# Performance work log

Hardware: AMD Instinct MI355X
Metric: run time of the kernel (lower is better)

## Reference

```python
import jax, jax.numpy as jnp
import numpy as np

B, S, DM = 4, 2048, 1024
H, HD = 16, 64  # num_heads, head_dimension


def setup_inputs() -> dict:
    key = jax.random.key(0)
    ks = jax.random.split(key, 11)
    s = 0.02
    return {
        "queries": jax.random.normal(ks[0], (B, S, DM), dtype=jnp.float32),
        "keys": jax.random.normal(ks[1], (B, S, DM), dtype=jnp.float32),
        "values": jax.random.normal(ks[2], (B, S, DM), dtype=jnp.float32),
        # projection params, stored [in, out] (transpose of torch Linear weight)
        "Wq": jax.random.normal(ks[3], (DM, H * HD), dtype=jnp.float32) * s,
        "bq": jnp.zeros((H * HD,), dtype=jnp.float32),
        "Wk": jax.random.normal(ks[4], (DM, H * HD), dtype=jnp.float32) * s,
        "bk": jnp.zeros((H * HD,), dtype=jnp.float32),
        "Wv": jax.random.normal(ks[5], (DM, H * HD), dtype=jnp.float32) * s,
        "bv": jnp.zeros((H * HD,), dtype=jnp.float32),
        "Wo": jax.random.normal(ks[6], (H * HD, DM), dtype=jnp.float32) * s,
        "bo": jnp.zeros((DM,), dtype=jnp.float32),
    }


def reference(queries, keys, values, Wq, bq, Wk, bk, Wv, bv, Wo, bo):
    b, s, _ = queries.shape
    # project and split heads: [b, s, H*HD] -> [b, H, s, HD]
    def split(x):
        return x.reshape(b, s, H, HD).transpose(0, 2, 1, 3)
    q = split(queries @ Wq + bq)
    k = split(keys @ Wk + bk)
    v = split(values @ Wv + bv)
    # raw scores [b, H, sq, sk]
    attn = jnp.einsum("bhqd,bhkd->bhqk", q, k)
    # FAITHFUL to source: mask is a no-op (masked_fill result discarded);
    # softmax over axis=2 (the QUERY axis), then scaled by 1/sqrt(HD) after.
    attn = jax.nn.softmax(attn, axis=2) / jnp.sqrt(jnp.float32(HD))
    out = jnp.einsum("bhqk,bhkd->bhqd", attn, v)  # [b, H, s, HD]
    out = out.transpose(0, 2, 1, 3).reshape(b, s, H * HD)
    return out @ Wo + bo
```

## Files before the change

### kernel.cpp

```cpp
#include <hip/hip_runtime.h>
#include <cstddef>


typedef unsigned short u16t;
typedef __attribute__((ext_vector_type(8))) short short8;
typedef __attribute__((ext_vector_type(4))) float floatx4;
typedef __attribute__((ext_vector_type(4))) unsigned int uintx4;

#define MFMA16(a, b, c) __builtin_amdgcn_mfma_f32_16x16x32_bf16((a), (b), (c), 0, 0, 0)
#define GLDS16(g, l)                                                        \
  __builtin_amdgcn_global_load_lds(                                         \
      (const __attribute__((address_space(1))) unsigned int*)(g),           \
      (__attribute__((address_space(3))) unsigned int*)(l), 16, 0, 0)

#if __has_builtin(__builtin_amdgcn_exp2f)
#define EXP2(x) __builtin_amdgcn_exp2f(x)
#else
#define EXP2(x) __expf(0.69314718f * (x))
#endif

static __device__ __forceinline__ u16t f2bf(float f) {
  union { float f; unsigned u; } v; v.f = f;
  unsigned r = v.u + 0x7FFFu + ((v.u >> 16) & 1u);
  return (u16t)(r >> 16);
}
static __device__ __forceinline__ unsigned pack2(float hi, float lo) {
  union { float f; unsigned u; } a, b; a.f = hi; b.f = lo;
  return __builtin_amdgcn_perm(a.u + 0x8000u, b.u + 0x8000u, 0x07060302u);
}

static __device__ __forceinline__ int swz(int row, int col) {
  return (((col >> 3) ^ (row & 7)) << 3) | (col & 7);
}

#define SEQ    2048
#define NHEAD  16
#define HDIM   64
#define DMODEL 1024

__global__ __launch_bounds__(256)
void wt_kernel(const float* __restrict__ W0, const float* __restrict__ W1,
               const float* __restrict__ W2, const float* __restrict__ W3,
               u16t* __restrict__ T0, u16t* __restrict__ T1,
               u16t* __restrict__ T2, u16t* __restrict__ T3) {
  int id = blockIdx.x * 256 + threadIdx.x;
  int wsel = id >> 17;
  int r = id & 131071;
  int n = r & 1023;
  int k0 = (r >> 10) << 3;
  const float* W = wsel == 0 ? W0 : wsel == 1 ? W1 : wsel == 2 ? W2 : W3;
  u16t* T = wsel == 0 ? T0 : wsel == 1 ? T1 : wsel == 2 ? T2 : T3;
  const float* src = W + (size_t)k0 * 1024 + n;
  float f[8];
#pragma unroll
  for (int i = 0; i < 8; ++i) f[i] = src[(size_t)i * 1024];
  uint4 p;
  p.x = pack2(f[1], f[0]); p.y = pack2(f[3], f[2]);
  p.z = pack2(f[5], f[4]); p.w = pack2(f[7], f[6]);
  *(uint4*)&T[(size_t)n * 1024 + (k0 & ~63) + swz(n, k0 & 63)] = p;
}

__global__ __launch_bounds__(256)
void cvt_kernel(const float* __restrict__ X0, const float* __restrict__ X1,
                u16t* __restrict__ T0, u16t* __restrict__ T1) {
  int id = blockIdx.x * 256 + threadIdx.x;
  int wsel = id >> 20;
  int r = id & 1048575;
  int m = r >> 7;
  int k0 = (r & 127) << 3;
  const float* X = wsel == 0 ? X0 : X1;
  u16t* T = wsel == 0 ? T0 : T1;
  const float4* src = (const float4*)(X + (size_t)m * 1024 + k0);
  float4 a = src[0], b = src[1];
  uint4 p;
  p.x = pack2(a.y, a.x); p.y = pack2(a.w, a.z);
  p.z = pack2(b.y, b.x); p.w = pack2(b.w, b.z);
  *(uint4*)&T[(size_t)m * 1024 + (k0 & ~63) + swz(m, k0 & 63)] = p;
}

template <int MODE>
__global__ __launch_bounds__(256)
void gemm_bt(const void* __restrict__ Ap0, const void* __restrict__ Ap1,
             const u16t* __restrict__ BT0, const u16t* __restrict__ BT1,
             const float* __restrict__ bias0, const float* __restrict__ bias1,
             void* __restrict__ Cp0, void* __restrict__ Cp1,
             float sc0, float sc1, const float* __restrict__ sscv) {
  constexpr int K = 1024;
  __shared__ __align__(16) u16t lA[128 * 64];
  __shared__ __align__(16) u16t lB[128 * 64];
  const int z = blockIdx.z;
  const void* Ap = z ? Ap1 : Ap0;
  const u16t* BT = z ? BT1 : BT0;
  const float* bias = z ? bias1 : bias0;
  void* Cp = z ? Cp1 : Cp0;
  const float qsc = z ? sc1 : sc0;
  const int tid = threadIdx.x;
  const int lane = tid & 63, w = tid >> 6;
  const int wm = w >> 1, wn = w & 1;
  const int lrow = lane & 15, lq = lane >> 4;
  const int raw = blockIdx.y * 8 + blockIdx.x;
  const int xcd = raw & 7, slot = raw >> 3;
  const int m0 = (xcd * 8 + (slot >> 3)) * 128;
  const int n0 = (slot & 7) * 128;

  floatx4 acc[4][4];
#pragma unroll
  for (int i = 0; i < 4; ++i)
#pragma unroll
    for (int j = 0; j < 4; ++j) acc[i][j] = {0.f, 0.f, 0.f, 0.f};

  for (int kb = 0; kb < K; kb += 64) {
    if constexpr (MODE == 2) {
      const float* Ag = (const float*)Ap;
#pragma unroll
      for (int i = 0; i < 8; ++i) {
        int e = (i * 256 + tid) * 4;
        int r = e >> 6, c = e & 63;
        const float* src = Ag + (size_t)(m0 + r) * K + kb + c;
        uint2 p;
        p.x = pack2(src[1], src[0]);
        p.y = pack2(src[3], src[2]);
        *(uint2*)&lA[r * 64 + swz(r, c)] = p;
      }
    } else {
      const u16t* Ag = (const u16t*)Ap;
#pragma unroll
      for (int i = 0; i < 4; ++i) {
        int chunk = w * 4 + i;
        int off = chunk * 1024 + lane * 16;
        int r = off >> 7, ib = off & 127;
        GLDS16(Ag + (size_t)(m0 + r) * K + kb + (ib >> 1), &lA[chunk * 512]);
      }
    }
#pragma unroll
    for (int i = 0; i < 4; ++i) {
      int chunk = w * 4 + i;
      int off = chunk * 1024 + lane * 16;
      int r = off >> 7, ib = off & 127;
      GLDS16(BT + (size_t)(n0 + r) * K + kb + (ib >> 1), &lB[chunk * 512]);
    }
    __syncthreads();
#pragma unroll
    for (int kk = 0; kk < 2; ++kk) {
      short8 af[4], bfr[4];
#pragma unroll
      for (int t = 0; t < 4; ++t) {
        int ar = wm * 64 + t * 16 + lrow;
        af[t] = *(const short8*)&lA[ar * 64 + swz(ar, kk * 32 + lq * 8)];
      }
#pragma unroll
      for (int t = 0; t < 4; ++t) {
        int br = wn * 64 + t * 16 + lrow;
        bfr[t] = *(const short8*)&lB[br * 64 + swz(br, kk * 32 + lq * 8)];
      }
#pragma unroll
      for (int i = 0; i < 4; ++i)
#pragma unroll
        for (int j = 0; j < 4; ++j)
          acc[i][j] = MFMA16(af[i], bfr[j], acc[i][j]);
    }
    __syncthreads();
  }

  float bvv[4];
#pragma unroll
  for (int j = 0; j < 4; ++j) bvv[j] = bias[n0 + wn * 64 + j * 16 + lrow];
  const int h = (n0 + wn * 64) >> 6;
#pragma unroll
  for (int i = 0; i < 4; ++i) {
#pragma unroll
    for (int r = 0; r < 4; ++r) {
      int rg = m0 + wm * 64 + i * 16 + lq * 4 + r;
      int b = rg >> 11, s = rg & 2047;
      float rs;
      if constexpr (MODE == 2) rs = sscv[(size_t)(b * NHEAD + h) * SEQ + s];
      else                     rs = qsc;
#pragma unroll
      for (int j = 0; j < 4; ++j) {
        int cg = n0 + wn * 64 + j * 16 + lrow;
        float v = acc[i][j][r] + bvv[j];
        if constexpr (MODE == 1) {
          ((float*)Cp)[(size_t)rg * 1024 + cg] = v;
        } else {
          v *= rs;
          int d = cg & 63;
          size_t bh = (size_t)(b * NHEAD + h);
          if constexpr (MODE == 0) {
            ((u16t*)Cp)[(bh * SEQ + s) * HDIM + swz(s, d)] = f2bf(v);
          } else {
            int sp = (s & ~31) | (((s >> 2) & 3) << 3) | (s & 3) |
                     (((s >> 4) & 1) << 2);
            ((u16t*)Cp)[(bh * HDIM + d) * SEQ + (s & ~127) + swz(d, sp & 127)] =
                f2bf(v);
          }
        }
      }
    }
  }
}

__global__ __launch_bounds__(256)
void stats_kernel(const u16t* __restrict__ Qb, const u16t* __restrict__ Kb,
                  float* __restrict__ ss) {
  __shared__ __align__(16) u16t lK[128 * 64];
  __shared__ __align__(16) u16t lQ[128 * 64];
  const int tid = threadIdx.x, lane = tid & 63, w = tid >> 6;
  const int lrow = lane & 15, lq = lane >> 4;
  const int bh = blockIdx.x;
  const int c0 = blockIdx.y * 128;
  const u16t* Kbase = Kb + (size_t)bh * (SEQ * HDIM);
  const u16t* Qbase = Qb + (size_t)bh * (SEQ * HDIM);

#pragma unroll
  for (int i = 0; i < 4; ++i) {
    int chunk = w * 4 + i;
    GLDS16(Kbase + (size_t)c0 * HDIM + chunk * 512 + lane * 8, &lK[chunk * 512]);
  }

  short8 bfK[4];
  float lcur[2] = {0.f, 0.f};

  for (int q0 = 0; q0 < SEQ; q0 += 128) {
#pragma unroll
    for (int i = 0; i < 4; ++i) {
      int chunk = w * 4 + i;
      GLDS16(Qbase + (size_t)q0 * HDIM + chunk * 512 + lane * 8, &lQ[chunk * 512]);
    }
    __syncthreads();
    if (q0 == 0) {
#pragma unroll
      for (int nt = 0; nt < 2; ++nt) {
        int kr = w * 32 + nt * 16 + lrow;
        bfK[nt * 2]     = *(const short8*)&lK[kr * 64 + swz(kr, lq * 8)];
        bfK[nt * 2 + 1] = *(const short8*)&lK[kr * 64 + swz(kr, lq * 8 + 32)];
      }
    }
#pragma unroll
    for (int mt = 0; mt < 8; ++mt) {
      int qr = mt * 16 + lrow;
      short8 af0 = *(const short8*)&lQ[qr * 64 + swz(qr, lq * 8)];
      short8 af1 = *(const short8*)&lQ[qr * 64 + swz(qr, lq * 8 + 32)];
#pragma unroll
      for (int nt = 0; nt < 2; ++nt) {
        floatx4 a = {0.f, 0.f, 0.f, 0.f};
        a = MFMA16(af0, bfK[nt * 2], a);
        a = MFMA16(af1, bfK[nt * 2 + 1], a);
        lcur[nt] += EXP2(a[0]) + EXP2(a[1]) + EXP2(a[2]) + EXP2(a[3]);
      }
    }
    __syncthreads();
  }
#pragma unroll
  for (int t = 0; t < 2; ++t) {
    float ll = lcur[t];
    ll += __shfl_xor(ll, 16);
    ll += __shfl_xor(ll, 32);
    lcur[t] = ll;
  }
  if (lane < 16) {
#pragma unroll
    for (int t = 0; t < 2; ++t) {
      int col = c0 + w * 32 + t * 16 + lane;
      ss[(size_t)bh * SEQ + col] = 1.f / (8.f * lcur[t]);
    }
  }
}

__global__ __launch_bounds__(256)
void attn_kernel(const u16t* __restrict__ Qb, const u16t* __restrict__ Kb,
                 const u16t* __restrict__ Vt, u16t* __restrict__ Hout) {
  __shared__ __align__(16) u16t lK[128 * 64];
  __shared__ __align__(16) u16t lV[64 * 128];
  const int tid = threadIdx.x, lane = tid & 63, w = tid >> 6;
  const int lrow = lane & 15, lq = lane >> 4;
  const int bh = blockIdx.x, q0 = blockIdx.y * 128;
  const size_t hb = (size_t)bh * (SEQ * HDIM);

#pragma unroll
  for (int i = 0; i < 4; ++i) {
    int chunk = w * 4 + i;
    GLDS16(Qb + hb + (size_t)q0 * HDIM + chunk * 512 + lane * 8, &lK[chunk * 512]);
  }
  __syncthreads();
  short8 bq[2][2];
#pragma unroll
  for (int j = 0; j < 2; ++j) {
    int qr = w * 32 + j * 16 + lrow;
    bq[j][0] = *(const short8*)&lK[qr * 64 + swz(qr, lq * 8)];
    bq[j][1] = *(const short8*)&lK[qr * 64 + swz(qr, lq * 8 + 32)];
  }
  __syncthreads();

  floatx4 ao[2][4];
#pragma unroll
  for (int j = 0; j < 2; ++j)
#pragma unroll
    for (int t = 0; t < 4; ++t) ao[j][t] = {0.f, 0.f, 0.f, 0.f};

  for (int kt = 0; kt < 16; ++kt) {
    const int k0 = kt * 128;
#pragma unroll
    for (int i = 0; i < 4; ++i) {
      int chunk = w * 4 + i;
      GLDS16(Kb + hb + (size_t)k0 * HDIM + chunk * 512 + lane * 8, &lK[chunk * 512]);
    }
#pragma unroll
    for (int i = 0; i < 4; ++i) {
      int chunk = w * 4 + i;
      int off = chunk * 1024 + lane * 16;
      int d = off >> 8, ib = off & 255;
      GLDS16(Vt + hb + ((size_t)d << 11) + k0 + (ib >> 1), &lV[chunk * 512]);
    }
    __syncthreads();

#pragma unroll
    for (int kw = 0; kw < 4; ++kw) {
      short8 ak[2][2];
#pragma unroll
      for (int t = 0; t < 2; ++t) {
        int kr = (kw * 2 + t) * 16 + lrow;
        ak[t][0] = *(const short8*)&lK[kr * 64 + swz(kr, lq * 8)];
        ak[t][1] = *(const short8*)&lK[kr * 64 + swz(kr, lq * 8 + 32)];
      }
      short8 pa[2];
#pragma unroll
      for (int j = 0; j < 2; ++j) {
        floatx4 s0 = {0.f, 0.f, 0.f, 0.f}, s1 = {0.f, 0.f, 0.f, 0.f};
        s0 = MFMA16(ak[0][0], bq[j][0], s0);
        s0 = MFMA16(ak[0][1], bq[j][1], s0);
        s1 = MFMA16(ak[1][0], bq[j][0], s1);
        s1 = MFMA16(ak[1][1], bq[j][1], s1);
        uintx4 pw;
        pw[0] = pack2(EXP2(s0[1]), EXP2(s0[0]));
        pw[1] = pack2(EXP2(s0[3]), EXP2(s0[2]));
        pw[2] = pack2(EXP2(s1[1]), EXP2(s1[0]));
        pw[3] = pack2(EXP2(s1[3]), EXP2(s1[2]));
        pa[j] = __builtin_bit_cast(short8, pw);
      }
#pragma unroll
      for (int dt = 0; dt < 4; ++dt) {
        int vr = dt * 16 + lrow;
        short8 bv = *(const short8*)&lV[vr * 128 + swz(vr, kw * 32 + lq * 8)];
        ao[0][dt] = MFMA16(pa[0], bv, ao[0][dt]);
        ao[1][dt] = MFMA16(pa[1], bv, ao[1][dt]);
      }
    }
    __syncthreads();
  }

  const int b = bh >> 4, h = bh & 15;
#pragma unroll
  for (int j = 0; j < 2; ++j)
#pragma unroll
    for (int dt = 0; dt < 4; ++dt) {
      int d = dt * 16 + lrow;
#pragma unroll
      for (int r = 0; r < 4; ++r) {
        int q = q0 + w * 32 + j * 16 + lq * 4 + r;
        Hout[((size_t)b * SEQ + q) * DMODEL + h * HDIM + swz(q, d)] = f2bf(ao[j][dt][r]);
      }
    }
}

extern "C" void kernel_launch(void* const* d_in, const int* in_sizes, int n_in,
                              void* d_out, int out_size, void* d_ws, size_t ws_size,
                              hipStream_t stream) {
  (void)in_sizes; (void)n_in; (void)out_size; (void)ws_size;
  const float* queries = (const float*)d_in[0];
  const float* keys    = (const float*)d_in[1];
  const float* values  = (const float*)d_in[2];
  const float* Wq = (const float*)d_in[3];
  const float* bq = (const float*)d_in[4];
  const float* Wk = (const float*)d_in[5];
  const float* bk = (const float*)d_in[6];
  const float* Wv = (const float*)d_in[7];
  const float* bv = (const float*)d_in[8];
  const float* Wo = (const float*)d_in[9];
  const float* bo = (const float*)d_in[10];

  char* ws = (char*)d_ws;
  const size_t MB = 1024 * 1024;
  u16t* Qb   = (u16t*)(ws + 0 * MB);
  u16t* Kb   = (u16t*)(ws + 16 * MB);
  u16t* qcv  = (u16t*)(ws + 32 * MB);
  u16t* Hout = qcv;
  u16t* kcv  = (u16t*)(ws + 48 * MB);
  u16t* Vt   = kcv;
  u16t* wqt  = (u16t*)(ws + 64 * MB);
  u16t* wkt  = (u16t*)(ws + 66 * MB);
  u16t* wvt  = (u16t*)(ws + 68 * MB);
  u16t* wot  = (u16t*)(ws + 70 * MB);
  float* ssc = (float*)(ws + 72 * MB);

  wt_kernel<<<2048, 256, 0, stream>>>(Wq, Wk, Wv, Wo, wqt, wkt, wvt, wot);

  cvt_kernel<<<8192, 256, 0, stream>>>(queries, keys, qcv, kcv);

  gemm_bt<0><<<dim3(8, 64, 2), 256, 0, stream>>>(
      qcv, kcv, wqt, wkt, bq, bk, Qb, Kb, 1.44269504f, 1.0f, nullptr);

  stats_kernel<<<dim3(64, 16), 256, 0, stream>>>(Qb, Kb, ssc);

  gemm_bt<2><<<dim3(8, 64, 1), 256, 0, stream>>>(
      values, values, wvt, wvt, bv, bv, Vt, Vt, 1.0f, 1.0f, ssc);

  attn_kernel<<<dim3(64, 16), 256, 0, stream>>>(Qb, Kb, Vt, Hout);

  gemm_bt<1><<<dim3(8, 64, 1), 256, 0, stream>>>(
      Hout, Hout, wot, wot, bo, bo, d_out, d_out, 1.0f, 1.0f, nullptr);
}
```

Before: 384.9 us.

## Double-buffer LDS tiles in stats and attention kernels, enlarge attention query tile

Both stats_kernel and attn_kernel now double-buffer their LDS tiles and prefetch two stages ahead. They use explicit vmcnt waits and raw barriers so global loads overlap with MFMA work. attn_kernel processes 256 queries per block instead of 128, which halves the grid, doubles K/V reuse per load and increases accumulator registers. MFMA sections get raised wave priority, and the bf16 packing uses the hardware v_cvt_pk_bf16_f32 instruction. The risks are lower occupancy from more LDS and registers, and fewer blocks to fill the CUs.

```diff
diff --git a/kernel.cpp b/kernel.cpp
--- a/kernel.cpp
+++ b/kernel.cpp
@@ -27,6 +27,11 @@
 static __device__ __forceinline__ unsigned pack2(float hi, float lo) {
   union { float f; unsigned u; } a, b; a.f = hi; b.f = lo;
   return __builtin_amdgcn_perm(a.u + 0x8000u, b.u + 0x8000u, 0x07060302u);
+}
+static __device__ __forceinline__ unsigned cvtpk(float lo, float hi) {
+  unsigned r;
+  asm("v_cvt_pk_bf16_f32 %0, %1, %2" : "=v"(r) : "v"(lo), "v"(hi));
+  return r;
 }
 
 static __device__ __forceinline__ int swz(int row, int col) {
@@ -202,8 +207,8 @@
 __global__ __launch_bounds__(256)
 void stats_kernel(const u16t* __restrict__ Qb, const u16t* __restrict__ Kb,
                   float* __restrict__ ss) {
-  __shared__ __align__(16) u16t lK[128 * 64];
-  __shared__ __align__(16) u16t lQ[128 * 64];
+  __shared__ __align__(16) u16t lK[8192];
+  __shared__ __align__(16) u16t lQ[2][8192];
   const int tid = threadIdx.x, lane = tid & 63, w = tid >> 6;
   const int lrow = lane & 15, lq = lane >> 4;
   const int bh = blockIdx.x;
@@ -211,44 +216,61 @@
   const u16t* Kbase = Kb + (size_t)bh * (SEQ * HDIM);
   const u16t* Qbase = Qb + (size_t)bh * (SEQ * HDIM);
 
+  auto stageQ = [&](int t) {
+    u16t* dst = lQ[t & 1];
+#pragma unroll
+    for (int i = 0; i < 4; ++i) {
+      int chunk = w * 4 + i;
+      GLDS16(Qbase + ((size_t)t << 13) + chunk * 512 + lane * 8, &dst[chunk * 512]);
+    }
+  };
+
 #pragma unroll
   for (int i = 0; i < 4; ++i) {
     int chunk = w * 4 + i;
     GLDS16(Kbase + (size_t)c0 * HDIM + chunk * 512 + lane * 8, &lK[chunk * 512]);
   }
+  stageQ(0);
+  stageQ(1);
+  asm volatile("s_waitcnt vmcnt(4)" ::: "memory");
+  __builtin_amdgcn_s_barrier();
 
   short8 bfK[4];
+#pragma unroll
+  for (int nt = 0; nt < 2; ++nt) {
+    int kr = w * 32 + nt * 16 + lrow;
+    bfK[nt * 2]     = *(const short8*)&lK[kr * 64 + swz(kr, lq * 8)];
+    bfK[nt * 2 + 1] = *(const short8*)&lK[kr * 64 + swz(kr, lq * 8 + 32)];
+  }
+
   float lcur[2] = {0.f, 0.f};
 
-  for (int q0 = 0; q0 < SEQ; q0 += 128) {
-#pragma unroll
-    for (int i = 0; i < 4; ++i) {
-      int chunk = w * 4 + i;
-      GLDS16(Qbase + (size_t)q0 * HDIM + chunk * 512 + lane * 8, &lQ[chunk * 512]);
-    }
-    __syncthreads();
-    if (q0 == 0) {
-#pragma unroll
-      for (int nt = 0; nt < 2; ++nt) {
-        int kr = w * 32 + nt * 16 + lrow;
-        bfK[nt * 2]     = *(const short8*)&lK[kr * 64 + swz(kr, lq * 8)];
-        bfK[nt * 2 + 1] = *(const short8*)&lK[kr * 64 + swz(kr, lq * 8 + 32)];
-      }
-    }
+#pragma unroll 2
+  for (int it = 0; it < 16; ++it) {
+    const u16t* Q_ = lQ[it & 1];
 #pragma unroll
     for (int mt = 0; mt < 8; ++mt) {
       int qr = mt * 16 + lrow;
-      short8 af0 = *(const short8*)&lQ[qr * 64 + swz(qr, lq * 8)];
-      short8 af1 = *(const short8*)&lQ[qr * 64 + swz(qr, lq * 8 + 32)];
+      short8 af0 = *(const short8*)&Q_[qr * 64 + swz(qr, lq * 8)];
+      short8 af1 = *(const short8*)&Q_[qr * 64 + swz(qr, lq * 8 + 32)];
 #pragma unroll
       for (int nt = 0; nt < 2; ++nt) {
         floatx4 a = {0.f, 0.f, 0.f, 0.f};
+        __builtin_amdgcn_s_setprio(1);
         a = MFMA16(af0, bfK[nt * 2], a);
         a = MFMA16(af1, bfK[nt * 2 + 1], a);
-        lcur[nt] += EXP2(a[0]) + EXP2(a[1]) + EXP2(a[2]) + EXP2(a[3]);
-      }
-    }
-    __syncthreads();
+        __builtin_amdgcn_s_setprio(0);
+        lcur[nt] += (EXP2(a[0]) + EXP2(a[1])) + (EXP2(a[2]) + EXP2(a[3]));
+      }
+    }
+    asm volatile("s_waitcnt lgkmcnt(0)" ::: "memory");
+    __builtin_amdgcn_s_barrier();
+    if (it < 14) stageQ(it + 2);
+    if (it < 15) {
+      if (it == 14) asm volatile("s_waitcnt vmcnt(0)" ::: "memory");
+      else          asm volatile("s_waitcnt vmcnt(4)" ::: "memory");
+      __builtin_amdgcn_s_barrier();
+    }
   }
 #pragma unroll
   for (int t = 0; t < 2; ++t) {
@@ -269,49 +291,63 @@
 __global__ __launch_bounds__(256)
 void attn_kernel(const u16t* __restrict__ Qb, const u16t* __restrict__ Kb,
                  const u16t* __restrict__ Vt, u16t* __restrict__ Hout) {
-  __shared__ __align__(16) u16t lK[128 * 64];
-  __shared__ __align__(16) u16t lV[64 * 128];
+  __shared__ __align__(16) u16t sK[2][8192];
+  __shared__ __align__(16) u16t sV[2][8192];
   const int tid = threadIdx.x, lane = tid & 63, w = tid >> 6;
   const int lrow = lane & 15, lq = lane >> 4;
-  const int bh = blockIdx.x, q0 = blockIdx.y * 128;
+  const int bh = blockIdx.x, q0 = blockIdx.y * 256;
   const size_t hb = (size_t)bh * (SEQ * HDIM);
 
-#pragma unroll
-  for (int i = 0; i < 4; ++i) {
-    int chunk = w * 4 + i;
-    GLDS16(Qb + hb + (size_t)q0 * HDIM + chunk * 512 + lane * 8, &lK[chunk * 512]);
-  }
-  __syncthreads();
-  short8 bq[2][2];
-#pragma unroll
-  for (int j = 0; j < 2; ++j) {
-    int qr = w * 32 + j * 16 + lrow;
-    bq[j][0] = *(const short8*)&lK[qr * 64 + swz(qr, lq * 8)];
-    bq[j][1] = *(const short8*)&lK[qr * 64 + swz(qr, lq * 8 + 32)];
-  }
-  __syncthreads();
-
-  floatx4 ao[2][4];
-#pragma unroll
-  for (int j = 0; j < 2; ++j)
-#pragma unroll
-    for (int t = 0; t < 4; ++t) ao[j][t] = {0.f, 0.f, 0.f, 0.f};
-
-  for (int kt = 0; kt < 16; ++kt) {
-    const int k0 = kt * 128;
+  auto stage = [&](int t) {
+    u16t* dK = sK[t & 1];
+    u16t* dV = sV[t & 1];
+    const int k0 = t << 7;
 #pragma unroll
     for (int i = 0; i < 4; ++i) {
       int chunk = w * 4 + i;
-      GLDS16(Kb + hb + (size_t)k0 * HDIM + chunk * 512 + lane * 8, &lK[chunk * 512]);
+      GLDS16(Kb + hb + (size_t)k0 * HDIM + chunk * 512 + lane * 8, &dK[chunk * 512]);
     }
 #pragma unroll
     for (int i = 0; i < 4; ++i) {
       int chunk = w * 4 + i;
       int off = chunk * 1024 + lane * 16;
       int d = off >> 8, ib = off & 255;
-      GLDS16(Vt + hb + ((size_t)d << 11) + k0 + (ib >> 1), &lV[chunk * 512]);
-    }
-    __syncthreads();
+      GLDS16(Vt + hb + ((size_t)d << 11) + k0 + (ib >> 1), &dV[chunk * 512]);
+    }
+  };
+
+  u16t* qs = (u16t*)sK;
+#pragma unroll
+  for (int i = 0; i < 8; ++i) {
+    int chunk = w * 8 + i;
+    GLDS16(Qb + hb + (size_t)q0 * HDIM + chunk * 512 + lane * 8, &qs[chunk * 512]);
+  }
+  __syncthreads();
+  short8 bq[4][2];
+#pragma unroll
+  for (int j = 0; j < 4; ++j) {
+    int qr = w * 64 + j * 16 + lrow;
+    bq[j][0] = *(const short8*)&qs[qr * 64 + swz(qr, lq * 8)];
+    bq[j][1] = *(const short8*)&qs[qr * 64 + swz(qr, lq * 8 + 32)];
+  }
+  __syncthreads();
+
+  floatx4 ao[4][4];
+#pragma unroll
+  for (int j = 0; j < 4; ++j)
+#pragma unroll
+    for (int t = 0; t < 4; ++t) ao[j][t] = {0.f, 0.f, 0.f, 0.f};
+
+  stage(0);
+  stage(1);
+
+#pragma unroll 2
+  for (int kt = 0; kt < 16; ++kt) {
+    if (kt < 15) asm volatile("s_waitcnt vmcnt(8)" ::: "memory");
+    else         asm volatile("s_waitcnt vmcnt(0)" ::: "memory");
+    __builtin_amdgcn_s_barrier();
+    const u16t* K_ = sK[kt & 1];
+    const u16t* V_ = sV[kt & 1];
 
 #pragma unroll
     for (int kw = 0; kw < 4; ++kw) {
@@ -319,44 +355,52 @@
 #pragma unroll
       for (int t = 0; t < 2; ++t) {
         int kr = (kw * 2 + t) * 16 + lrow;
-        ak[t][0] = *(const short8*)&lK[kr * 64 + swz(kr, lq * 8)];
-        ak[t][1] = *(const short8*)&lK[kr * 64 + swz(kr, lq * 8 + 32)];
-      }
-      short8 pa[2];
-#pragma unroll
-      for (int j = 0; j < 2; ++j) {
+        ak[t][0] = *(const short8*)&K_[kr * 64 + swz(kr, lq * 8)];
+        ak[t][1] = *(const short8*)&K_[kr * 64 + swz(kr, lq * 8 + 32)];
+      }
+      short8 pa[4];
+#pragma unroll
+      for (int j = 0; j < 4; ++j) {
         floatx4 s0 = {0.f, 0.f, 0.f, 0.f}, s1 = {0.f, 0.f, 0.f, 0.f};
+        __builtin_amdgcn_s_setprio(1);
         s0 = MFMA16(ak[0][0], bq[j][0], s0);
         s0 = MFMA16(ak[0][1], bq[j][1], s0);
         s1 = MFMA16(ak[1][0], bq[j][0], s1);
         s1 = MFMA16(ak[1][1], bq[j][1], s1);
+        __builtin_amdgcn_s_setprio(0);
         uintx4 pw;
-        pw[0] = pack2(EXP2(s0[1]), EXP2(s0[0]));
-        pw[1] = pack2(EXP2(s0[3]), EXP2(s0[2]));
-        pw[2] = pack2(EXP2(s1[1]), EXP2(s1[0]));
-        pw[3] = pack2(EXP2(s1[3]), EXP2(s1[2]));
+        pw[0] = cvtpk(EXP2(s0[0]), EXP2(s0[1]));
+        pw[1] = cvtpk(EXP2(s0[2]), EXP2(s0[3]));
+        pw[2] = cvtpk(EXP2(s1[0]), EXP2(s1[1]));
+        pw[3] = cvtpk(EXP2(s1[2]), EXP2(s1[3]));
         pa[j] = __builtin_bit_cast(short8, pw);
       }
+      __builtin_amdgcn_s_setprio(1);
 #pragma unroll
       for (int dt = 0; dt < 4; ++dt) {
         int vr = dt * 16 + lrow;
-        short8 bv = *(const short8*)&lV[vr * 128 + swz(vr, kw * 32 + lq * 8)];
-        ao[0][dt] = MFMA16(pa[0], bv, ao[0][dt]);
-        ao[1][dt] = MFMA16(pa[1], bv, ao[1][dt]);
-      }
-    }
-    __syncthreads();
+        short8 bv = *(const short8*)&V_[vr * 128 + swz(vr, kw * 32 + lq * 8)];
+#pragma unroll
+        for (int j = 0; j < 4; ++j)
+          ao[j][dt] = MFMA16(pa[j], bv, ao[j][dt]);
+      }
+      __builtin_amdgcn_s_setprio(0);
+    }
+
+    asm volatile("s_waitcnt lgkmcnt(0)" ::: "memory");
+    __builtin_amdgcn_s_barrier();
+    if (kt < 14) stage(kt + 2);
   }
 
   const int b = bh >> 4, h = bh & 15;
 #pragma unroll
-  for (int j = 0; j < 2; ++j)
+  for (int j = 0; j < 4; ++j)
 #pragma unroll
     for (int dt = 0; dt < 4; ++dt) {
       int d = dt * 16 + lrow;
 #pragma unroll
       for (int r = 0; r < 4; ++r) {
-        int q = q0 + w * 32 + j * 16 + lq * 4 + r;
+        int q = q0 + w * 64 + j * 16 + lq * 4 + r;
         Hout[((size_t)b * SEQ + q) * DMODEL + h * HDIM + swz(q, d)] = f2bf(ao[j][dt][r]);
       }
     }
@@ -404,7 +448,7 @@
   gemm_bt<2><<<dim3(8, 64, 1), 256, 0, stream>>>(
       values, values, wvt, wvt, bv, bv, Vt, Vt, 1.0f, 1.0f, ssc);
 
-  attn_kernel<<<dim3(64, 16), 256, 0, stream>>>(Qb, Kb, Vt, Hout);
+  attn_kernel<<<dim3(64, 8), 256, 0, stream>>>(Qb, Kb, Vt, Hout);
 
   gemm_bt<1><<<dim3(8, 64, 1), 256, 0, stream>>>(
       Hout, Hout, wot, wot, bo, bo, d_out, d_out, 1.0f, 1.0f, nullptr);
```

After: 400.5 us. +4.0%, slower.
